# Performance work log

Measured on AMD Instinct MI355X. Metric: run time of the kernel, lower is better.

## Reference

```python
import jax, jax.numpy as jnp
import numpy as np

N = 8192
NODE_DIM = 512
HIDDEN = 256
N_CLASSES = 16
N_EDGES = 262144


def build_adj_mat(edge_index, n):
    # Dense {0,1} adjacency from COO edge list, plus self-loops so every
    # row of the masked softmax has at least one finite entry.
    adj = jnp.zeros((n, n), dtype=jnp.float32)
    adj = adj.at[edge_index[0], edge_index[1]].set(1.0)
    diag = jnp.arange(n)
    adj = adj.at[diag, diag].set(1.0)
    return adj


def setup_inputs() -> dict:
    key = jax.random.key(0)
    k_x, k_e, k_W, k_a1, k_a2, k_fw, k_fb = jax.random.split(key, 7)
    x = jax.random.normal(k_x, (N, NODE_DIM), dtype=jnp.float32)
    edge_index = jax.random.randint(k_e, (2, N_EDGES), 0, N, dtype=jnp.int64)
    # xavier_uniform-style inits
    def xavier(k, shape):
        fan_in, fan_out = shape[1], shape[0]
        lim = float(np.sqrt(6.0 / (fan_in + fan_out)))
        return jax.random.uniform(k, shape, jnp.float32, -lim, lim)
    W = xavier(k_W, (HIDDEN, NODE_DIM))
    a1 = xavier(k_a1, (HIDDEN, 1))
    a2 = xavier(k_a2, (HIDDEN, 1))
    fc_w = xavier(k_fw, (N_CLASSES, HIDDEN))
    fc_b = jnp.zeros((N_CLASSES,), dtype=jnp.float32)
    return {"x": x, "edge_index": edge_index, "W": W, "a1": a1, "a2": a2,
            "fc_w": fc_w, "fc_b": fc_b}


def reference(x, edge_index, W, a1, a2, fc_w, fc_b):
    adj = build_adj_mat(edge_index, x.shape[0])
    h = x @ W.T                                   # [N, H]
    f1 = (h @ a1)[:, 0]                           # [N]
    f2 = (h @ a2)[:, 0]                           # [N]
    e = jax.nn.leaky_relu(f1[:, None] + f2[None, :], negative_slope=0.01)
    e = e * adj
    e = jnp.where(e == 0, -jnp.inf, e)            # mask non-edges (and exact zeros, as in source)
    alpha = jax.nn.softmax(e, axis=1)             # [N, N]
    out = jax.nn.elu(alpha @ h)                   # [N, H]
    logits = out @ fc_w.T + fc_b                  # [N, n_classes]
    return logits
```

## Files before the change

kernel.cpp:

```cpp
#include <hip/hip_runtime.h>
#include <hip/hip_bf16.h>
#include <stdint.h>
#include <math.h>

#define N_NODES 8192
#define NDIM    512
#define HID     256
#define NCLS    16
#define NE      262144
#define MWR     256
#define CAP     128

static __device__ __forceinline__ ushort f2bf(float f) {
    uint32_t u = __float_as_uint(f);
    uint32_t r = (u + 0x7FFFu + ((u >> 16) & 1u)) >> 16;
    return (ushort)r;
}
static __device__ __forceinline__ float bf2f(ushort u) {
    return __uint_as_float(((uint32_t)u) << 16);
}
static __device__ __forceinline__ void wave_lds_fence() {
    asm volatile("s_waitcnt lgkmcnt(0)" ::: "memory");
}

__global__ __launch_bounds__(256) void build_mask(const void* __restrict__ edges,
                                                  uint32_t* __restrict__ mask) {
    const long long* p64 = (const long long*)edges;
    long long probe = p64[threadIdx.x & 31];
    const int is32 = __any(probe < 0 || probe >= (long long)N_NODES);

    int idx = blockIdx.x * blockDim.x + threadIdx.x;
    if (idx < NE) {
        int src, dst;
        if (is32) {
            const int* p = (const int*)edges;
            src = p[idx]; dst = p[NE + idx];
        } else {
            src = (int)p64[idx]; dst = (int)p64[NE + idx];
        }
        atomicOr(&mask[src * MWR + (dst >> 5)], 1u << (dst & 31));
    } else {
        int d = idx - NE;
        if (d < N_NODES) atomicOr(&mask[d * MWR + (d >> 5)], 1u << (d & 31));
    }
}

__global__ __launch_bounds__(256) void gemm_h(const float* __restrict__ x,
                                              const float* __restrict__ W,
                                              const float* __restrict__ a1,
                                              const float* __restrict__ a2,
                                              ushort* __restrict__ hb,
                                              float* __restrict__ f1,
                                              float* __restrict__ f2) {
    __shared__ float xs[32][68];
    __shared__ float ws[32][68];
    const int tid  = threadIdx.x;
    const int row0 = blockIdx.y * 64;
    const int col0 = blockIdx.x * 64;
    const int lr = tid >> 3;
    const int lc = (tid & 7) << 2;
    const int tx = tid & 15;
    const int ty = tid >> 4;
    float acc[4][4] = {};
    const float* xp = x + (size_t)(row0 + lr) * NDIM + lc;
    const float* wp = W + (size_t)(col0 + lr) * NDIM + lc;

    for (int k0 = 0; k0 < NDIM; k0 += 32) {
        float4 xa = *(const float4*)(xp + k0);
        float4 xb = *(const float4*)(xp + k0 + 32 * NDIM);
        float4 wa = *(const float4*)(wp + k0);
        float4 wb = *(const float4*)(wp + k0 + 32 * NDIM);
        __syncthreads();
        xs[lc + 0][lr] = xa.x; xs[lc + 1][lr] = xa.y; xs[lc + 2][lr] = xa.z; xs[lc + 3][lr] = xa.w;
        xs[lc + 0][lr + 32] = xb.x; xs[lc + 1][lr + 32] = xb.y; xs[lc + 2][lr + 32] = xb.z; xs[lc + 3][lr + 32] = xb.w;
        ws[lc + 0][lr] = wa.x; ws[lc + 1][lr] = wa.y; ws[lc + 2][lr] = wa.z; ws[lc + 3][lr] = wa.w;
        ws[lc + 0][lr + 32] = wb.x; ws[lc + 1][lr + 32] = wb.y; ws[lc + 2][lr + 32] = wb.z; ws[lc + 3][lr + 32] = wb.w;
        __syncthreads();
        #pragma unroll
        for (int kk = 0; kk < 32; ++kk) {
            float4 a = *(const float4*)&xs[kk][ty << 2];
            float4 b = *(const float4*)&ws[kk][tx << 2];
            acc[0][0] += a.x * b.x; acc[0][1] += a.x * b.y; acc[0][2] += a.x * b.z; acc[0][3] += a.x * b.w;
            acc[1][0] += a.y * b.x; acc[1][1] += a.y * b.y; acc[1][2] += a.y * b.z; acc[1][3] += a.y * b.w;
            acc[2][0] += a.z * b.x; acc[2][1] += a.z * b.y; acc[2][2] += a.z * b.z; acc[2][3] += a.z * b.w;
            acc[3][0] += a.w * b.x; acc[3][1] += a.w * b.y; acc[3][2] += a.w * b.z; acc[3][3] += a.w * b.w;
        }
    }
    const float4 a1c = *(const float4*)&a1[col0 + (tx << 2)];
    const float4 a2c = *(const float4*)&a2[col0 + (tx << 2)];
    #pragma unroll
    for (int i = 0; i < 4; ++i) {
        const int r = row0 + (ty << 2) + i;
        ushort4 hv;
        hv.x = f2bf(acc[i][0]); hv.y = f2bf(acc[i][1]);
        hv.z = f2bf(acc[i][2]); hv.w = f2bf(acc[i][3]);
        *(ushort4*)&hb[(size_t)r * HID + col0 + (tx << 2)] = hv;
        float p1 = acc[i][0] * a1c.x + acc[i][1] * a1c.y + acc[i][2] * a1c.z + acc[i][3] * a1c.w;
        float p2 = acc[i][0] * a2c.x + acc[i][1] * a2c.y + acc[i][2] * a2c.z + acc[i][3] * a2c.w;
        #pragma unroll
        for (int msk = 8; msk; msk >>= 1) {
            p1 += __shfl_xor(p1, msk);
            p2 += __shfl_xor(p2, msk);
        }
        if (tx == 0) {
            atomicAdd(&f1[r], p1);
            atomicAdd(&f2[r], p2);
        }
    }
}

__global__ __launch_bounds__(256) void aggregate(const uint32_t* __restrict__ mask,
                                                 const ushort* __restrict__ hb,
                                                 const float* __restrict__ f1,
                                                 const float* __restrict__ f2,
                                                 const float* __restrict__ fc_w,
                                                 const float* __restrict__ fc_b,
                                                 float* __restrict__ out) {
    __shared__ int   sh_j[4][CAP];
    __shared__ float sh_v[4][CAP];
    __shared__ float sh_o[4][HID];
    __shared__ int   sh_cnt[4];

    const int wv   = threadIdx.x >> 6;
    const int lane = threadIdx.x & 63;
    const int row  = blockIdx.x * 4 + wv;
    int*   jl = sh_j[wv];
    float* vl = sh_v[wv];
    float* ol = sh_o[wv];

    if (lane == 0) sh_cnt[wv] = 0;

    const float fi = f1[row];
    uint4 mw = *(const uint4*)&mask[(size_t)row * MWR + lane * 4];

    float m = -INFINITY, s = 0.f;
    #pragma unroll
    for (int wi = 0; wi < 4; ++wi) {
        uint32_t w = (&mw.x)[wi];
        while (w) {
            int b = __ffs(w) - 1;
            w &= w - 1;
            int j = (lane * 4 + wi) * 32 + b;
            float z = fi + f2[j];
            float v = z > 0.f ? z : 0.01f * z;
            if (v != 0.f) {
                int slot = atomicAdd(&sh_cnt[wv], 1);
                if (slot < CAP) { jl[slot] = j; vl[slot] = v; }
                if (v > m) { s = s * __expf(m - v) + 1.f; m = v; }
                else       { s += __expf(v - m); }
            }
        }
    }
    float M = m;
    #pragma unroll
    for (int off = 32; off; off >>= 1) M = fmaxf(M, __shfl_xor(M, off));
    float S = (m == -INFINITY) ? 0.f : s * __expf(m - M);
    #pragma unroll
    for (int off = 32; off; off >>= 1) S += __shfl_xor(S, off);

    const int cnt = min(sh_cnt[wv], CAP);
    wave_lds_fence();

    const float inv = 1.f / S;
    for (int n = lane; n < cnt; n += 64) vl[n] = __expf(vl[n] - M) * inv;
    wave_lds_fence();

    float a0 = 0.f, a1v = 0.f, a2v = 0.f, a3 = 0.f;
    const ushort* hcol = hb + lane * 4;
    int n = 0;
    for (; n + 4 <= cnt; n += 4) {
        #pragma unroll
        for (int u = 0; u < 4; ++u) {
            int j   = jl[n + u];
            float v = vl[n + u];
            ushort4 hv = *(const ushort4*)(hcol + (size_t)j * HID);
            a0 += v * bf2f(hv.x); a1v += v * bf2f(hv.y);
            a2v += v * bf2f(hv.z); a3 += v * bf2f(hv.w);
        }
    }
    for (; n < cnt; ++n) {
        int j   = jl[n];
        float v = vl[n];
        ushort4 hv = *(const ushort4*)(hcol + (size_t)j * HID);
        a0 += v * bf2f(hv.x); a1v += v * bf2f(hv.y);
        a2v += v * bf2f(hv.z); a3 += v * bf2f(hv.w);
    }
    float4 e;
    e.x = a0  > 0.f ? a0  : expm1f(a0);
    e.y = a1v > 0.f ? a1v : expm1f(a1v);
    e.z = a2v > 0.f ? a2v : expm1f(a2v);
    e.w = a3  > 0.f ? a3  : expm1f(a3);
    *(float4*)&ol[lane * 4] = e;
    wave_lds_fence();

    const int c = lane >> 2;
    const int q = lane & 3;
    float p = 0.f;
    #pragma unroll
    for (int i = 0; i < 64; i += 4) {
        float4 o = *(const float4*)&ol[q * 64 + i];
        float4 w = *(const float4*)&fc_w[c * HID + q * 64 + i];
        p += o.x * w.x + o.y * w.y + o.z * w.z + o.w * w.w;
    }
    p += __shfl_xor(p, 1);
    p += __shfl_xor(p, 2);
    if (q == 0) out[(size_t)row * NCLS + c] = p + fc_b[c];
}

extern "C" void kernel_launch(void* const* d_in, const int* in_sizes, int n_in,
                              void* d_out, int out_size, void* d_ws, size_t ws_size,
                              hipStream_t stream) {
    const float* x    = (const float*)d_in[0];
    const void*  ei   = d_in[1];
    const float* W    = (const float*)d_in[2];
    const float* a1   = (const float*)d_in[3];
    const float* a2   = (const float*)d_in[4];
    const float* fc_w = (const float*)d_in[5];
    const float* fc_b = (const float*)d_in[6];
    float* out = (float*)d_out;

    char* ws = (char*)d_ws;
    uint32_t* mask = (uint32_t*)ws;
    float*    f1   = (float*)(ws + 8388608);
    float*    f2   = (float*)(ws + 8388608 + 32768);
    ushort*   hb   = (ushort*)(ws + 8388608 + 65536);

    hipMemsetAsync(ws, 0, 8388608 + 65536, stream);
    const int total = NE + N_NODES;
    build_mask<<<(total + 255) / 256, 256, 0, stream>>>(ei, mask);
    gemm_h<<<dim3(HID / 64, N_NODES / 64), 256, 0, stream>>>(x, W, a1, a2, hb, f1, f2);
    aggregate<<<N_NODES / 4, 256, 0, stream>>>(mask, hb, f1, f2, fc_w, fc_b, out);
}
```

Measured before the change: 151.9 us.

## Use split-bf16 MFMA for the feature projection GEMM

Replaces the scalar FP32 tiled GEMM computing h = x W^T with bf16 MFMA instructions. Each FP32 operand is split into hi/lo bf16 parts, and three MFMAs per tile approximate FP32 accuracy. Operands go into a 64-wide K tile in XOR-swizzled LDS, and the launch grid is remapped with a block swizzle. The aim is to cut the FP32 FMA cost of the 8192x512x256 GEMM, at the price of extra conversion work and a small loss of precision from dropping the lo*lo term.

```diff
diff --git a/kernel.cpp b/kernel.cpp
--- a/kernel.cpp
+++ b/kernel.cpp
@@ -10,6 +10,9 @@
 #define NE      262144
 #define MWR     256
 #define CAP     128
+
+typedef __attribute__((ext_vector_type(8))) short short8;
+typedef __attribute__((ext_vector_type(4))) float f32x4;
 
 static __device__ __forceinline__ ushort f2bf(float f) {
     uint32_t u = __float_as_uint(f);
@@ -52,59 +55,108 @@
                                               ushort* __restrict__ hb,
                                               float* __restrict__ f1,
                                               float* __restrict__ f2) {
-    __shared__ float xs[32][68];
-    __shared__ float ws[32][68];
+    __shared__ ushort lds[4][64 * 64];
+
     const int tid  = threadIdx.x;
-    const int row0 = blockIdx.y * 64;
-    const int col0 = blockIdx.x * 64;
-    const int lr = tid >> 3;
-    const int lc = (tid & 7) << 2;
-    const int tx = tid & 15;
-    const int ty = tid >> 4;
-    float acc[4][4] = {};
-    const float* xp = x + (size_t)(row0 + lr) * NDIM + lc;
-    const float* wp = W + (size_t)(col0 + lr) * NDIM + lc;
-
-    for (int k0 = 0; k0 < NDIM; k0 += 32) {
-        float4 xa = *(const float4*)(xp + k0);
-        float4 xb = *(const float4*)(xp + k0 + 32 * NDIM);
-        float4 wa = *(const float4*)(wp + k0);
-        float4 wb = *(const float4*)(wp + k0 + 32 * NDIM);
+    const int lane = tid & 63;
+    const int wv   = tid >> 6;
+    const int wr   = wv >> 1;
+    const int wc   = wv & 1;
+    const int cl   = lane & 15;
+    const int rg   = lane >> 4;
+
+    const int bid  = blockIdx.x;
+    const int swz  = (bid & 7) * 64 + (bid >> 3);
+    const int row0 = (swz >> 2) * 64;
+    const int col0 = (swz & 3) * 64;
+
+    const int tr  = tid >> 4;
+    const int tc4 = (tid & 15) << 2;
+
+    f32x4 acc[2][2] = {};
+
+    for (int k0 = 0; k0 < NDIM; k0 += 64) {
+        float4 av[4], bv[4];
+        #pragma unroll
+        for (int it = 0; it < 4; ++it) {
+            av[it] = *(const float4*)&x[(size_t)(row0 + tr + it * 16) * NDIM + k0 + tc4];
+            bv[it] = *(const float4*)&W[(size_t)(col0 + tr + it * 16) * NDIM + k0 + tc4];
+        }
         __syncthreads();
-        xs[lc + 0][lr] = xa.x; xs[lc + 1][lr] = xa.y; xs[lc + 2][lr] = xa.z; xs[lc + 3][lr] = xa.w;
-        xs[lc + 0][lr + 32] = xb.x; xs[lc + 1][lr + 32] = xb.y; xs[lc + 2][lr + 32] = xb.z; xs[lc + 3][lr + 32] = xb.w;
-        ws[lc + 0][lr] = wa.x; ws[lc + 1][lr] = wa.y; ws[lc + 2][lr] = wa.z; ws[lc + 3][lr] = wa.w;
-        ws[lc + 0][lr + 32] = wb.x; ws[lc + 1][lr + 32] = wb.y; ws[lc + 2][lr + 32] = wb.z; ws[lc + 3][lr + 32] = wb.w;
+        #pragma unroll
+        for (int it = 0; it < 4; ++it) {
+            const int r   = tr + it * 16;
+            const int idx = (r * 64 + tc4) ^ ((r & 7) << 3);
+            ushort4 hi, lo;
+            hi.x = f2bf(av[it].x); lo.x = f2bf(av[it].x - bf2f(hi.x));
+            hi.y = f2bf(av[it].y); lo.y = f2bf(av[it].y - bf2f(hi.y));
+            hi.z = f2bf(av[it].z); lo.z = f2bf(av[it].z - bf2f(hi.z));
+            hi.w = f2bf(av[it].w); lo.w = f2bf(av[it].w - bf2f(hi.w));
+            *(ushort4*)&lds[0][idx] = hi;
+            *(ushort4*)&lds[1][idx] = lo;
+            hi.x = f2bf(bv[it].x); lo.x = f2bf(bv[it].x - bf2f(hi.x));
+            hi.y = f2bf(bv[it].y); lo.y = f2bf(bv[it].y - bf2f(hi.y));
+            hi.z = f2bf(bv[it].z); lo.z = f2bf(bv[it].z - bf2f(hi.z));
+            hi.w = f2bf(bv[it].w); lo.w = f2bf(bv[it].w - bf2f(hi.w));
+            *(ushort4*)&lds[2][idx] = hi;
+            *(ushort4*)&lds[3][idx] = lo;
+        }
         __syncthreads();
-        #pragma unroll
-        for (int kk = 0; kk < 32; ++kk) {
-            float4 a = *(const float4*)&xs[kk][ty << 2];
-            float4 b = *(const float4*)&ws[kk][tx << 2];
-            acc[0][0] += a.x * b.x; acc[0][1] += a.x * b.y; acc[0][2] += a.x * b.z; acc[0][3] += a.x * b.w;
-            acc[1][0] += a.y * b.x; acc[1][1] += a.y * b.y; acc[1][2] += a.y * b.z; acc[1][3] += a.y * b.w;
-            acc[2][0] += a.z * b.x; acc[2][1] += a.z * b.y; acc[2][2] += a.z * b.z; acc[2][3] += a.z * b.w;
-            acc[3][0] += a.w * b.x; acc[3][1] += a.w * b.y; acc[3][2] += a.w * b.z; acc[3][3] += a.w * b.w;
-        }
-    }
-    const float4 a1c = *(const float4*)&a1[col0 + (tx << 2)];
-    const float4 a2c = *(const float4*)&a2[col0 + (tx << 2)];
-    #pragma unroll
-    for (int i = 0; i < 4; ++i) {
-        const int r = row0 + (ty << 2) + i;
-        ushort4 hv;
-        hv.x = f2bf(acc[i][0]); hv.y = f2bf(acc[i][1]);
-        hv.z = f2bf(acc[i][2]); hv.w = f2bf(acc[i][3]);
-        *(ushort4*)&hb[(size_t)r * HID + col0 + (tx << 2)] = hv;
-        float p1 = acc[i][0] * a1c.x + acc[i][1] * a1c.y + acc[i][2] * a1c.z + acc[i][3] * a1c.w;
-        float p2 = acc[i][0] * a2c.x + acc[i][1] * a2c.y + acc[i][2] * a2c.z + acc[i][3] * a2c.w;
-        #pragma unroll
-        for (int msk = 8; msk; msk >>= 1) {
-            p1 += __shfl_xor(p1, msk);
-            p2 += __shfl_xor(p2, msk);
-        }
-        if (tx == 0) {
-            atomicAdd(&f1[r], p1);
-            atomicAdd(&f2[r], p2);
+
+        #pragma unroll
+        for (int ks = 0; ks < 2; ++ks) {
+            short8 ah[2], al[2], bh[2], bl[2];
+            const int ka = ks * 32 + rg * 8;
+            #pragma unroll
+            for (int i = 0; i < 2; ++i) {
+                const int ra = wr * 32 + i * 16 + cl;
+                const int ia = (ra * 64 + ka) ^ ((ra & 7) << 3);
+                ah[i] = *(short8*)&lds[0][ia];
+                al[i] = *(short8*)&lds[1][ia];
+                const int rb = wc * 32 + i * 16 + cl;
+                const int ib = (rb * 64 + ka) ^ ((rb & 7) << 3);
+                bh[i] = *(short8*)&lds[2][ib];
+                bl[i] = *(short8*)&lds[3][ib];
+            }
+            #pragma unroll
+            for (int mi = 0; mi < 2; ++mi)
+                #pragma unroll
+                for (int ni = 0; ni < 2; ++ni) {
+                    acc[mi][ni] = __builtin_amdgcn_mfma_f32_16x16x32_bf16(ah[mi], bh[ni], acc[mi][ni], 0, 0, 0);
+                    acc[mi][ni] = __builtin_amdgcn_mfma_f32_16x16x32_bf16(ah[mi], bl[ni], acc[mi][ni], 0, 0, 0);
+                    acc[mi][ni] = __builtin_amdgcn_mfma_f32_16x16x32_bf16(al[mi], bh[ni], acc[mi][ni], 0, 0, 0);
+                }
+        }
+    }
+
+    float a1c[2], a2c[2];
+    #pragma unroll
+    for (int ni = 0; ni < 2; ++ni) {
+        const int c = col0 + wc * 32 + ni * 16 + cl;
+        a1c[ni] = a1[c];
+        a2c[ni] = a2[c];
+    }
+    #pragma unroll
+    for (int mi = 0; mi < 2; ++mi) {
+        #pragma unroll
+        for (int reg = 0; reg < 4; ++reg) {
+            const int r = row0 + wr * 32 + mi * 16 + rg * 4 + reg;
+            float p1 = 0.f, p2 = 0.f;
+            #pragma unroll
+            for (int ni = 0; ni < 2; ++ni) {
+                const float v = acc[mi][ni][reg];
+                hb[(size_t)r * HID + col0 + wc * 32 + ni * 16 + cl] = f2bf(v);
+                p1 += v * a1c[ni];
+                p2 += v * a2c[ni];
+            }
+            p1 += __shfl_xor(p1, 1); p1 += __shfl_xor(p1, 2);
+            p1 += __shfl_xor(p1, 4); p1 += __shfl_xor(p1, 8);
+            p2 += __shfl_xor(p2, 1); p2 += __shfl_xor(p2, 2);
+            p2 += __shfl_xor(p2, 4); p2 += __shfl_xor(p2, 8);
+            if (cl == 0) {
+                atomicAdd(&f1[r], p1);
+                atomicAdd(&f2[r], p2);
+            }
         }
     }
 }
@@ -228,6 +280,6 @@
     hipMemsetAsync(ws, 0, 8388608 + 65536, stream);
     const int total = NE + N_NODES;
     build_mask<<<(total + 255) / 256, 256, 0, stream>>>(ei, mask);
-    gemm_h<<<dim3(HID / 64, N_NODES / 64), 256, 0, stream>>>(x, W, a1, a2, hb, f1, f2);
+    gemm_h<<<512, 256, 0, stream>>>(x, W, a1, a2, hb, f1, f2);
     aggregate<<<N_NODES / 4, 256, 0, stream>>>(mask, hb, f1, f2, fc_w, fc_b, out);
 }
```

After: 133.5 us. 1.14x faster.
